# Optimization experiments

Measured on AMD Instinct MI355X. Metric: run time of the kernel, lower is better.

The kernel has to match this reference:

```python
import jax, jax.numpy as jnp
import numpy as np
import math

E_IN, E_OUT = 512, 96
B, QL, PL = 64, 128, 196

def _lin(k, shape):
    fan_in = shape[1]
    bound = 1.0 / math.sqrt(fan_in)
    k1, k2 = jax.random.split(k)
    W = jax.random.uniform(k1, shape, jnp.float32, -bound, bound)
    b = jax.random.uniform(k2, (shape[0],), jnp.float32, -bound, bound)
    return W, b

def setup_inputs() -> dict:
    key = jax.random.key(0)
    ks = jax.random.split(key, 16)
    inp = {
        'z_d_cls': jax.random.normal(ks[0], (B, E_IN), jnp.float32),
        'Z_d_tok': jax.random.normal(ks[1], (B, QL, E_IN), jnp.float32),
        'z_t_cls': jax.random.normal(ks[2], (B, E_IN), jnp.float32),
        'Z_t_tok': jax.random.normal(ks[3], (B, QL, E_IN), jnp.float32),
        'z_v_cls': jax.random.normal(ks[4], (B, E_IN), jnp.float32),
        'Z_v_patch': jax.random.normal(ks[5], (B, PL, E_IN), jnp.float32),
    }
    names = ['t_cls', 'd_cls', 'v_cls', 't_tok', 'v_patch', 'tgl_q', 'tgl_k', 'tgl_v']
    for i, n in enumerate(names):
        W, b = _lin(ks[6 + i], (E_OUT, E_IN))
        inp[f'W_{n}'] = W
        inp[f'b_{n}'] = b
    inp['ln_g'] = jnp.ones((E_OUT,), jnp.float32)
    inp['ln_b'] = jnp.zeros((E_OUT,), jnp.float32)
    return inp

def _l2n(x, eps=1e-6):
    return x / jnp.maximum(jnp.linalg.norm(x, axis=-1, keepdims=True), eps)

def _proj(x, W, b):
    return x @ W.T + b

def _layer_norm(x, g, b, eps=1e-5):
    mu = jnp.mean(x, axis=-1, keepdims=True)
    var = jnp.mean((x - mu) ** 2, axis=-1, keepdims=True)
    return (x - mu) / jnp.sqrt(var + eps) * g + b

def reference(z_d_cls, Z_d_tok, z_t_cls, Z_t_tok, z_v_cls, Z_v_patch,
              W_t_cls, b_t_cls, W_d_cls, b_d_cls, W_v_cls, b_v_cls,
              W_t_tok, b_t_tok, W_v_patch, b_v_patch,
              W_tgl_q, b_tgl_q, W_tgl_k, b_tgl_k, W_tgl_v, b_tgl_v,
              ln_g, ln_b):
    # --- TGG: global-global text/doc cosine sim [B, B]
    t = _l2n(_proj(z_t_cls, W_t_cls, b_t_cls))
    d = _l2n(_proj(z_d_cls, W_d_cls, b_d_cls))
    S_TGG = t @ d.T
    # --- TGL: cross-attention over all batch pairs
    Q = _proj(Z_d_tok, W_tgl_q, b_tgl_q)   # [b, q, h]
    K = _proj(Z_t_tok, W_tgl_k, b_tgl_k)   # [c, k, h]
    V = _proj(Z_t_tok, W_tgl_v, b_tgl_v)   # [c, k, h]
    scores = jnp.einsum('bqh,ckh->bcqk', Q, K) / math.sqrt(E_OUT)
    attn = jax.nn.softmax(scores, axis=-1)
    context = jnp.einsum('bcqk,ckh->bcqh', attn, V).mean(axis=2)  # [b, c, h]
    context = _layer_norm(context, ln_g, ln_b)
    S_TGL = jnp.einsum('ih,ijh->ij', d, _l2n(context))
    S_TIB = 0.5 * (S_TGG + S_TGL)
    # --- CGG: global-global text/vision cosine sim
    v = _l2n(_proj(z_v_cls, W_v_cls, b_v_cls))
    S_CGG = t @ v.T
    # --- CLL: token-patch max similarity
    t_tok = _l2n(_proj(Z_t_tok, W_t_tok, b_t_tok))        # [b, t, h]
    v_pat = _l2n(_proj(Z_v_patch, W_v_patch, b_v_patch))  # [c, p, h]
    sim = jnp.einsum('bth,cph->bctp', t_tok, v_pat)
    S_CLL = sim.max(axis=(-1, -2))
    S_CAB = 0.5 * (S_CGG + S_CLL)
    return S_TIB + S_CAB
```

## Files before the change

### kernel.cpp

```cpp
#include <hip/hip_runtime.h>
#include <hip/hip_bf16.h>
#include <math.h>

typedef __bf16 bf16;
typedef __attribute__((ext_vector_type(8))) __bf16 bf16x8;
typedef __attribute__((ext_vector_type(2))) float f32x2;
typedef __attribute__((ext_vector_type(4))) float f32x4;
typedef __attribute__((ext_vector_type(4))) unsigned int uint4v;

#define MFMA16(a, b, c) __builtin_amdgcn_mfma_f32_16x16x32_bf16(a, b, c, 0, 0, 0)

#define QSCALE 0.14724450f

__device__ inline bf16x8 cvt8(const float* p) {
    f32x4 lo = *(const f32x4*)p;
    f32x4 hi = *(const f32x4*)(p + 4);
    bf16x8 r;
    r[0] = (bf16)lo[0]; r[1] = (bf16)lo[1]; r[2] = (bf16)lo[2]; r[3] = (bf16)lo[3];
    r[4] = (bf16)hi[0]; r[5] = (bf16)hi[1]; r[6] = (bf16)hi[2]; r[7] = (bf16)hi[3];
    return r;
}


struct WPtrs { const float* W[8]; };

__global__ __launch_bounds__(256) void cvtw_kernel(WPtrs wp, bf16* __restrict__ Wb) {
    int j   = blockIdx.x / 48;
    int blk = blockIdx.x - j * 48;
    int idx = (blk * 256 + threadIdx.x) * 4;
    f32x4 v = *(const f32x4*)(wp.W[j] + idx);
    bf16* dst = Wb + j * 49152 + idx;
    dst[0] = (bf16)v[0]; dst[1] = (bf16)v[1]; dst[2] = (bf16)v[2]; dst[3] = (bf16)v[3];
}


struct ProjParams {
    const float* src[8];
    const float* B[8];
    void* dst[8];
    const bf16* Wb;
};

__global__ __launch_bounds__(256) void proj_kernel(ProjParams p) {
    int g   = blockIdx.x;
    int tid = threadIdx.x;
    int w2 = tid >> 6;
    int nh = w2 & 1, kh = w2 >> 1;
    int lane = tid & 63;
    int m = lane & 15, quad = lane >> 4;

    int job = 0, base = 0;
    if (g >= 2)    { job = 1; base = 2; }
    if (g >= 4)    { job = 2; base = 4; }
    if (g >= 6)    { job = 3; base = 6; }
    if (g >= 262)  { job = 4; base = 262; }
    if (g >= 518)  { job = 5; base = 518; }
    if (g >= 774)  { job = 6; base = 774; }
    if (g >= 1030) { job = 7; base = 1030; }
    int r0 = (g - base) << 5;

    const float* X  = p.src[job];
    const bf16*  wb = p.Wb + job * 49152 + (size_t)(nh * 48 + m) * 512 + kh * 256 + quad * 8;
    const float* x0 = X + (size_t)(r0 + m) * 512 + kh * 256 + quad * 8;
    const float* x1 = x0 + 16 * 512;

    f32x4 acc[2][3] = {};
    #pragma unroll
    for (int kk = 0; kk < 256; kk += 32) {
        bf16x8 a0 = cvt8(x0 + kk);
        bf16x8 a1 = cvt8(x1 + kk);
        #pragma unroll
        for (int nt = 0; nt < 3; nt++) {
            bf16x8 b = *(const bf16x8*)(wb + nt * 8192 + kk);
            acc[0][nt] = MFMA16(a0, b, acc[0][nt]);
            acc[1][nt] = MFMA16(a1, b, acc[1][nt]);
        }
    }

    __shared__ float red[2 * 64 * 24];
    __shared__ float sx[2][2][16];
    float* myred = red + (nh * 64 + lane) * 24;
    if (kh) {
        #pragma unroll
        for (int t2 = 0; t2 < 2; t2++)
            #pragma unroll
            for (int nt = 0; nt < 3; nt++)
                *(f32x4*)(myred + (t2 * 3 + nt) * 4) = acc[t2][nt];
    }
    __syncthreads();

    bool norm = (job < 3) || (job >= 6);
    const float* Bv = p.B[job];
    if (!kh) {
        #pragma unroll
        for (int t2 = 0; t2 < 2; t2++)
            #pragma unroll
            for (int nt = 0; nt < 3; nt++) {
                f32x4 o = *(const f32x4*)(myred + (t2 * 3 + nt) * 4);
                float bb = Bv[nh * 48 + nt * 16 + m];
                acc[t2][nt][0] += o[0] + bb; acc[t2][nt][1] += o[1] + bb;
                acc[t2][nt][2] += o[2] + bb; acc[t2][nt][3] += o[3] + bb;
            }
        if (norm) {
            float ss[2][4];
            #pragma unroll
            for (int t2 = 0; t2 < 2; t2++)
                #pragma unroll
                for (int r = 0; r < 4; r++) {
                    float s = 0.0f;
                    #pragma unroll
                    for (int nt = 0; nt < 3; nt++) s += acc[t2][nt][r] * acc[t2][nt][r];
                    s += __shfl_xor(s, 1); s += __shfl_xor(s, 2);
                    s += __shfl_xor(s, 4); s += __shfl_xor(s, 8);
                    ss[t2][r] = s;
                }
            if (m == 0) {
                #pragma unroll
                for (int t2 = 0; t2 < 2; t2++)
                    #pragma unroll
                    for (int r = 0; r < 4; r++)
                        sx[nh][t2][quad * 4 + r] = ss[t2][r];
            }
        }
    }
    __syncthreads();
    if (!kh) {
        if (norm) {
            #pragma unroll
            for (int t2 = 0; t2 < 2; t2++)
                #pragma unroll
                for (int r = 0; r < 4; r++) {
                    float s = 0.0f;
                    #pragma unroll
                    for (int nt = 0; nt < 3; nt++) s += acc[t2][nt][r] * acc[t2][nt][r];
                    s += __shfl_xor(s, 1); s += __shfl_xor(s, 2);
                    s += __shfl_xor(s, 4); s += __shfl_xor(s, 8);
                    float tot = s + sx[1 - nh][t2][quad * 4 + r];
                    float inv = 1.0f / fmaxf(sqrtf(tot), 1e-6f);
                    #pragma unroll
                    for (int nt = 0; nt < 3; nt++) acc[t2][nt][r] *= inv;
                }
        } else if (job == 3) {
            #pragma unroll
            for (int t2 = 0; t2 < 2; t2++)
                #pragma unroll
                for (int nt = 0; nt < 3; nt++) {
                    acc[t2][nt][0] *= QSCALE; acc[t2][nt][1] *= QSCALE;
                    acc[t2][nt][2] *= QSCALE; acc[t2][nt][3] *= QSCALE;
                }
        }
        if (job < 3) {
            float* dst = (float*)p.dst[job];
            #pragma unroll
            for (int t2 = 0; t2 < 2; t2++)
                #pragma unroll
                for (int r = 0; r < 4; r++)
                    #pragma unroll
                    for (int nt = 0; nt < 3; nt++)
                        dst[(size_t)(r0 + t2 * 16 + quad * 4 + r) * 96 + nh * 48 + nt * 16 + m] = acc[t2][nt][r];
        } else {
            bf16* dst = (bf16*)p.dst[job];
            #pragma unroll
            for (int t2 = 0; t2 < 2; t2++)
                #pragma unroll
                for (int r = 0; r < 4; r++)
                    #pragma unroll
                    for (int nt = 0; nt < 3; nt++)
                        dst[(size_t)(r0 + t2 * 16 + quad * 4 + r) * 96 + nh * 48 + nt * 16 + m] = (bf16)acc[t2][nt][r];
        }
    }
}


__global__ __launch_bounds__(256) void attn_kernel(
    const bf16* __restrict__ Qg, const bf16* __restrict__ Kg, const bf16* __restrict__ Vg,
    float* __restrict__ Ctx)
{
    int b  = blockIdx.x >> 4;
    int cg = blockIdx.x & 15;
    int tid = threadIdx.x, lane = tid & 63, w = tid >> 6;
    int m = lane & 15, quad = lane >> 4;
    const bf16* Q = Qg + (size_t)b * (128 * 96);

    bf16x8 qa0[3], qa1[3];
    #pragma unroll
    for (int i = 0; i < 3; i++) {
        qa0[i] = *(const bf16x8*)(Q + (size_t)(w * 32 + m) * 96 + i * 32 + quad * 8);
        qa1[i] = *(const bf16x8*)(Q + (size_t)(w * 32 + 16 + m) * 96 + i * 32 + quad * 8);
    }

    __shared__ __align__(16) bf16 Klds[128 * 104];
    __shared__ float wsum4[4][128];
    __shared__ float wk[128];
    __shared__ float ctxp[4][96];

    for (int ci = 0; ci < 4; ci++) {
        int c = cg * 4 + ci;
        const bf16* K = Kg + (size_t)c * (128 * 96);
        const bf16* V = Vg + (size_t)c * (128 * 96);
        #pragma unroll
        for (int it = 0; it < 6; it++) {
            int ch = it * 256 + tid;
            int row = ch / 12, seg = ch - row * 12;
            *(uint4v*)(Klds + row * 104 + seg * 8) = *(const uint4v*)(K + ch * 8);
        }
        __syncthreads();

        f32x4 acc[2][8] = {};
        #pragma unroll
        for (int kki = 0; kki < 3; kki++) {
            #pragma unroll
            for (int nt = 0; nt < 8; nt++) {
                bf16x8 bb = *(const bf16x8*)(Klds + (nt * 16 + m) * 104 + kki * 32 + quad * 8);
                acc[0][nt] = MFMA16(qa0[kki], bb, acc[0][nt]);
                acc[1][nt] = MFMA16(qa1[kki], bb, acc[1][nt]);
            }
        }
        float wpart[8];
        #pragma unroll
        for (int nt = 0; nt < 8; nt++) wpart[nt] = 0.0f;
        #pragma unroll
        for (int mt = 0; mt < 2; mt++) {
            #pragma unroll
            for (int r = 0; r < 4; r++) {
                float tv[8]; float s = 0.0f;
                #pragma unroll
                for (int nt = 0; nt < 8; nt++) { tv[nt] = exp2f(acc[mt][nt][r]); s += tv[nt]; }
                s += __shfl_xor(s, 1); s += __shfl_xor(s, 2);
                s += __shfl_xor(s, 4); s += __shfl_xor(s, 8);
                float inv = 1.0f / s;
                #pragma unroll
                for (int nt = 0; nt < 8; nt++) wpart[nt] += tv[nt] * inv;
            }
        }
        #pragma unroll
        for (int nt = 0; nt < 8; nt++) {
            wpart[nt] += __shfl_xor(wpart[nt], 16);
            wpart[nt] += __shfl_xor(wpart[nt], 32);
        }
        if (lane < 16) {
            #pragma unroll
            for (int nt = 0; nt < 8; nt++) wsum4[w][nt * 16 + lane] = wpart[nt];
        }
        __syncthreads();
        if (tid < 128) wk[tid] = wsum4[0][tid] + wsum4[1][tid] + wsum4[2][tid] + wsum4[3][tid];
        __syncthreads();
        {
            float c0 = 0.0f, c1 = 0.0f;
            if (lane < 48) {
                #pragma unroll 4
                for (int r = 0; r < 32; r++) {
                    int k = w * 32 + r;
                    unsigned u = *(const unsigned*)(V + (size_t)k * 96 + lane * 2);
                    float lo = __uint_as_float(u << 16);
                    float hi = __uint_as_float(u & 0xffff0000u);
                    float wkk = wk[k];
                    c0 += wkk * lo; c1 += wkk * hi;
                }
                ctxp[w][lane * 2]     = c0;
                ctxp[w][lane * 2 + 1] = c1;
            }
        }
        __syncthreads();
        if (tid < 96)
            Ctx[(size_t)(b * 64 + c) * 96 + tid] =
                (ctxp[0][tid] + ctxp[1][tid] + ctxp[2][tid] + ctxp[3][tid]) * (1.0f / 128.0f);
    }
}


__global__ __launch_bounds__(256) void cll_kernel(
    const bf16* __restrict__ Tt, const bf16* __restrict__ Vp, float* __restrict__ S_CLL)
{
    int c = blockIdx.x >> 3, bg = blockIdx.x & 7;
    int tid = threadIdx.x, lane = tid & 63, w = tid >> 6;
    int m = lane & 15, quad = lane >> 4;
    const bf16* P = Vp + (size_t)c * (196 * 96);

    __shared__ __align__(16) bf16 Plds[196 * 104];
    __shared__ float red[8][4];
    for (int ch = tid; ch < 2352; ch += 256) {
        int row = ch / 12, seg = ch - row * 12;
        *(uint4v*)(Plds + row * 104 + seg * 8) = *(const uint4v*)(P + ch * 8);
    }
    int rofs[13];
    #pragma unroll
    for (int nt = 0; nt < 13; nt++) {
        int r = nt * 16 + m; if (r > 195) r = 195;
        rofs[nt] = r * 104;
    }
    __syncthreads();

    for (int bi = 0; bi < 8; bi++) {
        const bf16* T = Tt + (size_t)(bg * 8 + bi) * (128 * 96);
        f32x4 acc[2][13] = {};
        #pragma unroll
        for (int kk = 0; kk < 96; kk += 32) {
            bf16x8 a0 = *(const bf16x8*)(T + (size_t)(w * 32 + m) * 96 + kk + quad * 8);
            bf16x8 a1 = *(const bf16x8*)(T + (size_t)(w * 32 + 16 + m) * 96 + kk + quad * 8);
            #pragma unroll
            for (int nt = 0; nt < 13; nt++) {
                bf16x8 bb = *(const bf16x8*)(Plds + rofs[nt] + kk + quad * 8);
                acc[0][nt] = MFMA16(a0, bb, acc[0][nt]);
                acc[1][nt] = MFMA16(a1, bb, acc[1][nt]);
            }
        }
        float mx = -3.4e38f;
        #pragma unroll
        for (int mt = 0; mt < 2; mt++)
            #pragma unroll
            for (int nt = 0; nt < 13; nt++)
                #pragma unroll
                for (int r = 0; r < 4; r++) mx = fmaxf(mx, acc[mt][nt][r]);
        #pragma unroll
        for (int d = 1; d < 64; d <<= 1) mx = fmaxf(mx, __shfl_xor(mx, d));
        if (lane == 0) red[bi][w] = mx;
    }
    __syncthreads();
    if (tid < 8)
        S_CLL[(size_t)(bg * 8 + tid) * 64 + c] =
            fmaxf(fmaxf(red[tid][0], red[tid][1]), fmaxf(red[tid][2], red[tid][3]));
}


__global__ __launch_bounds__(256) void epi_kernel(
    const float* __restrict__ Ctx, const float* __restrict__ t, const float* __restrict__ d,
    const float* __restrict__ v, const float* __restrict__ S_CLL,
    const float* __restrict__ ln_g, const float* __restrict__ ln_b,
    float* __restrict__ out)
{
    int pr = blockIdx.x * 4 + (threadIdx.x >> 6);
    int lane = threadIdx.x & 63;
    int i = pr >> 6, j = pr & 63;
    bool act = lane < 48;

    float c0 = 0, c1 = 0, t0 = 0, t1 = 0;
    float dj0 = 0, dj1 = 0, di0 = 0, di1 = 0, v0 = 0, v1 = 0, g0 = 0, g1 = 0, bb0 = 0, bb1 = 0;
    if (act) {
        f32x2 cc  = *(const f32x2*)(Ctx + (size_t)pr * 96 + lane * 2);
        f32x2 tt  = *(const f32x2*)(t + i * 96 + lane * 2);
        f32x2 ddj = *(const f32x2*)(d + j * 96 + lane * 2);
        f32x2 ddi = *(const f32x2*)(d + i * 96 + lane * 2);
        f32x2 vv  = *(const f32x2*)(v + j * 96 + lane * 2);
        f32x2 gg  = *(const f32x2*)(ln_g + lane * 2);
        f32x2 bbv = *(const f32x2*)(ln_b + lane * 2);
        c0 = cc[0]; c1 = cc[1]; t0 = tt[0]; t1 = tt[1];
        dj0 = ddj[0]; dj1 = ddj[1]; di0 = ddi[0]; di1 = ddi[1];
        v0 = vv[0]; v1 = vv[1];
        g0 = gg[0]; g1 = gg[1]; bb0 = bbv[0]; bb1 = bbv[1];
    }
    float s = c0 + c1;
    #pragma unroll
    for (int k = 1; k < 64; k <<= 1) s += __shfl_xor(s, k);
    float mean = s * (1.0f / 96.0f);
    float e0 = act ? (c0 - mean) : 0.0f;
    float e1 = act ? (c1 - mean) : 0.0f;
    float q = e0 * e0 + e1 * e1;
    #pragma unroll
    for (int k = 1; k < 64; k <<= 1) q += __shfl_xor(q, k);
    float rstd = rsqrtf(q * (1.0f / 96.0f) + 1e-5f);
    float y0 = act ? (e0 * rstd * g0 + bb0) : 0.0f;
    float y1 = act ? (e1 * rstd * g1 + bb1) : 0.0f;
    float dot = y0 * di0 + y1 * di1;
    float ssq = y0 * y0 + y1 * y1;
    float tg  = t0 * dj0 + t1 * dj1;
    float cg  = t0 * v0 + t1 * v1;
    #pragma unroll
    for (int k = 1; k < 64; k <<= 1) {
        dot += __shfl_xor(dot, k); ssq += __shfl_xor(ssq, k);
        tg  += __shfl_xor(tg, k);  cg  += __shfl_xor(cg, k);
    }
    if (lane == 0) {
        float stgl = dot / fmaxf(sqrtf(ssq), 1e-6f);
        out[pr] = 0.5f * (tg + stgl) + 0.5f * (cg + S_CLL[pr]);
    }
}


extern "C" void kernel_launch(void* const* d_in, const int* in_sizes, int n_in,
                              void* d_out, int out_size, void* d_ws, size_t ws_size,
                              hipStream_t stream)
{
    (void)in_sizes; (void)n_in; (void)out_size; (void)ws_size;
    char* ws = (char*)d_ws;
    float* t     = (float*)(ws + 0);
    float* d     = (float*)(ws + 24576);
    float* v     = (float*)(ws + 49152);
    float* S_CLL = (float*)(ws + 90112);
    bf16* Wb = (bf16*)(ws + 106496);
    bf16* Qb = (bf16*)(ws + 892928);
    bf16* Kb = (bf16*)(ws + 892928 + 1572864);
    bf16* Vb = (bf16*)(ws + 892928 + 2 * 1572864);
    bf16* Tt = (bf16*)(ws + 892928 + 3 * 1572864);
    bf16* Vp = (bf16*)(ws + 892928 + 4 * 1572864);
    float* Ctx = (float*)(ws + 892928 + 4 * 1572864 + 2408448);

    WPtrs wp;
    wp.W[0] = (const float*)d_in[6];
    wp.W[1] = (const float*)d_in[8];
    wp.W[2] = (const float*)d_in[10];
    wp.W[3] = (const float*)d_in[16];
    wp.W[4] = (const float*)d_in[18];
    wp.W[5] = (const float*)d_in[20];
    wp.W[6] = (const float*)d_in[12];
    wp.W[7] = (const float*)d_in[14];
    hipLaunchKernelGGL(cvtw_kernel, dim3(384), dim3(256), 0, stream, wp, Wb);

    ProjParams pp;
    pp.Wb = Wb;
    pp.src[0] = (const float*)d_in[2];  pp.B[0] = (const float*)d_in[7];  pp.dst[0] = t;
    pp.src[1] = (const float*)d_in[0];  pp.B[1] = (const float*)d_in[9];  pp.dst[1] = d;
    pp.src[2] = (const float*)d_in[4];  pp.B[2] = (const float*)d_in[11]; pp.dst[2] = v;
    pp.src[3] = (const float*)d_in[1];  pp.B[3] = (const float*)d_in[17]; pp.dst[3] = Qb;
    pp.src[4] = (const float*)d_in[3];  pp.B[4] = (const float*)d_in[19]; pp.dst[4] = Kb;
    pp.src[5] = (const float*)d_in[3];  pp.B[5] = (const float*)d_in[21]; pp.dst[5] = Vb;
    pp.src[6] = (const float*)d_in[3];  pp.B[6] = (const float*)d_in[13]; pp.dst[6] = Tt;
    pp.src[7] = (const float*)d_in[5];  pp.B[7] = (const float*)d_in[15]; pp.dst[7] = Vp;
    hipLaunchKernelGGL(proj_kernel, dim3(1422), dim3(256), 0, stream, pp);

    hipLaunchKernelGGL(attn_kernel, dim3(1024), dim3(256), 0, stream,
                       (const bf16*)Qb, (const bf16*)Kb, (const bf16*)Vb, Ctx);
    hipLaunchKernelGGL(cll_kernel, dim3(512), dim3(256), 0, stream,
                       (const bf16*)Tt, (const bf16*)Vp, S_CLL);
    hipLaunchKernelGGL(epi_kernel, dim3(1024), dim3(256), 0, stream,
                       (const float*)Ctx, (const float*)t, (const float*)d, (const float*)v,
                       (const float*)S_CLL, (const float*)d_in[22], (const float*)d_in[23],
                       (float*)d_out);
}
```

Measured before the change: 260.2 us.

## Split attention grid to one block per pair and fuse epilogue into CLL kernel

The attention kernel now launches one block per (b,c) pair, 4096 blocks instead of 1024 blocks each looping over four c values. This spreads the work across more blocks to raise parallelism, at the cost of reloading Q fragments per block. The epilogue kernel is folded into the CLL kernel, so S_CLL stays in shared memory and one launch plus a global round trip is removed. Each CLL block now also does layer norm and the final combination for its eight output pairs.

```diff
diff --git a/kernel.cpp b/kernel.cpp
--- a/kernel.cpp
+++ b/kernel.cpp
@@ -176,101 +176,96 @@
     const bf16* __restrict__ Qg, const bf16* __restrict__ Kg, const bf16* __restrict__ Vg,
     float* __restrict__ Ctx)
 {
-    int b  = blockIdx.x >> 4;
-    int cg = blockIdx.x & 15;
+    int pr = blockIdx.x;
+    int b = pr >> 6, c = pr & 63;
     int tid = threadIdx.x, lane = tid & 63, w = tid >> 6;
     int m = lane & 15, quad = lane >> 4;
     const bf16* Q = Qg + (size_t)b * (128 * 96);
-
-    bf16x8 qa0[3], qa1[3];
-    #pragma unroll
-    for (int i = 0; i < 3; i++) {
-        qa0[i] = *(const bf16x8*)(Q + (size_t)(w * 32 + m) * 96 + i * 32 + quad * 8);
-        qa1[i] = *(const bf16x8*)(Q + (size_t)(w * 32 + 16 + m) * 96 + i * 32 + quad * 8);
-    }
+    const bf16* K = Kg + (size_t)c * (128 * 96);
+    const bf16* V = Vg + (size_t)c * (128 * 96);
 
     __shared__ __align__(16) bf16 Klds[128 * 104];
+    #pragma unroll
+    for (int it = 0; it < 6; it++) {
+        int ch = it * 256 + tid;
+        int row = ch / 12, seg = ch - row * 12;
+        *(uint4v*)(Klds + row * 104 + seg * 8) = *(const uint4v*)(K + ch * 8);
+    }
+    __syncthreads();
+
+    f32x4 acc[2][8] = {};
+    #pragma unroll
+    for (int kk = 0; kk < 96; kk += 32) {
+        bf16x8 a0 = *(const bf16x8*)(Q + (size_t)(w * 32 + m) * 96 + kk + quad * 8);
+        bf16x8 a1 = *(const bf16x8*)(Q + (size_t)(w * 32 + 16 + m) * 96 + kk + quad * 8);
+        #pragma unroll
+        for (int nt = 0; nt < 8; nt++) {
+            bf16x8 bb = *(const bf16x8*)(Klds + (nt * 16 + m) * 104 + kk + quad * 8);
+            acc[0][nt] = MFMA16(a0, bb, acc[0][nt]);
+            acc[1][nt] = MFMA16(a1, bb, acc[1][nt]);
+        }
+    }
+    float wpart[8];
+    #pragma unroll
+    for (int nt = 0; nt < 8; nt++) wpart[nt] = 0.0f;
+    #pragma unroll
+    for (int mt = 0; mt < 2; mt++) {
+        #pragma unroll
+        for (int r = 0; r < 4; r++) {
+            float tv[8]; float s = 0.0f;
+            #pragma unroll
+            for (int nt = 0; nt < 8; nt++) { tv[nt] = exp2f(acc[mt][nt][r]); s += tv[nt]; }
+            s += __shfl_xor(s, 1); s += __shfl_xor(s, 2);
+            s += __shfl_xor(s, 4); s += __shfl_xor(s, 8);
+            float inv = 1.0f / s;
+            #pragma unroll
+            for (int nt = 0; nt < 8; nt++) wpart[nt] += tv[nt] * inv;
+        }
+    }
+    #pragma unroll
+    for (int nt = 0; nt < 8; nt++) {
+        wpart[nt] += __shfl_xor(wpart[nt], 16);
+        wpart[nt] += __shfl_xor(wpart[nt], 32);
+    }
     __shared__ float wsum4[4][128];
     __shared__ float wk[128];
     __shared__ float ctxp[4][96];
-
-    for (int ci = 0; ci < 4; ci++) {
-        int c = cg * 4 + ci;
-        const bf16* K = Kg + (size_t)c * (128 * 96);
-        const bf16* V = Vg + (size_t)c * (128 * 96);
-        #pragma unroll
-        for (int it = 0; it < 6; it++) {
-            int ch = it * 256 + tid;
-            int row = ch / 12, seg = ch - row * 12;
-            *(uint4v*)(Klds + row * 104 + seg * 8) = *(const uint4v*)(K + ch * 8);
-        }
-        __syncthreads();
-
-        f32x4 acc[2][8] = {};
-        #pragma unroll
-        for (int kki = 0; kki < 3; kki++) {
-            #pragma unroll
-            for (int nt = 0; nt < 8; nt++) {
-                bf16x8 bb = *(const bf16x8*)(Klds + (nt * 16 + m) * 104 + kki * 32 + quad * 8);
-                acc[0][nt] = MFMA16(qa0[kki], bb, acc[0][nt]);
-                acc[1][nt] = MFMA16(qa1[kki], bb, acc[1][nt]);
+    if (lane < 16) {
+        #pragma unroll
+        for (int nt = 0; nt < 8; nt++) wsum4[w][nt * 16 + lane] = wpart[nt];
+    }
+    __syncthreads();
+    if (tid < 128) wk[tid] = wsum4[0][tid] + wsum4[1][tid] + wsum4[2][tid] + wsum4[3][tid];
+    __syncthreads();
+    {
+        float c0 = 0.0f, c1 = 0.0f;
+        if (lane < 48) {
+            #pragma unroll 4
+            for (int r = 0; r < 32; r++) {
+                int k = w * 32 + r;
+                unsigned u = *(const unsigned*)(V + (size_t)k * 96 + lane * 2);
+                float lo = __uint_as_float(u << 16);
+                float hi = __uint_as_float(u & 0xffff0000u);
+                float wkk = wk[k];
+                c0 += wkk * lo; c1 += wkk * hi;
             }
-        }
-        float wpart[8];
-        #pragma unroll
-        for (int nt = 0; nt < 8; nt++) wpart[nt] = 0.0f;
-        #pragma unroll
-        for (int mt = 0; mt < 2; mt++) {
-            #pragma unroll
-            for (int r = 0; r < 4; r++) {
-                float tv[8]; float s = 0.0f;
-                #pragma unroll
-                for (int nt = 0; nt < 8; nt++) { tv[nt] = exp2f(acc[mt][nt][r]); s += tv[nt]; }
-                s += __shfl_xor(s, 1); s += __shfl_xor(s, 2);
-                s += __shfl_xor(s, 4); s += __shfl_xor(s, 8);
-                float inv = 1.0f / s;
-                #pragma unroll
-                for (int nt = 0; nt < 8; nt++) wpart[nt] += tv[nt] * inv;
-            }
-        }
-        #pragma unroll
-        for (int nt = 0; nt < 8; nt++) {
-            wpart[nt] += __shfl_xor(wpart[nt], 16);
-            wpart[nt] += __shfl_xor(wpart[nt], 32);
-        }
-        if (lane < 16) {
-            #pragma unroll
-            for (int nt = 0; nt < 8; nt++) wsum4[w][nt * 16 + lane] = wpart[nt];
-        }
-        __syncthreads();
-        if (tid < 128) wk[tid] = wsum4[0][tid] + wsum4[1][tid] + wsum4[2][tid] + wsum4[3][tid];
-        __syncthreads();
-        {
-            float c0 = 0.0f, c1 = 0.0f;
-            if (lane < 48) {
-                #pragma unroll 4
-                for (int r = 0; r < 32; r++) {
-                    int k = w * 32 + r;
-                    unsigned u = *(const unsigned*)(V + (size_t)k * 96 + lane * 2);
-                    float lo = __uint_as_float(u << 16);
-                    float hi = __uint_as_float(u & 0xffff0000u);
-                    float wkk = wk[k];
-                    c0 += wkk * lo; c1 += wkk * hi;
-                }
-                ctxp[w][lane * 2]     = c0;
-                ctxp[w][lane * 2 + 1] = c1;
-            }
-        }
-        __syncthreads();
-        if (tid < 96)
-            Ctx[(size_t)(b * 64 + c) * 96 + tid] =
-                (ctxp[0][tid] + ctxp[1][tid] + ctxp[2][tid] + ctxp[3][tid]) * (1.0f / 128.0f);
-    }
+            ctxp[w][lane * 2]     = c0;
+            ctxp[w][lane * 2 + 1] = c1;
+        }
+    }
+    __syncthreads();
+    if (tid < 96)
+        Ctx[(size_t)pr * 96 + tid] =
+            (ctxp[0][tid] + ctxp[1][tid] + ctxp[2][tid] + ctxp[3][tid]) * (1.0f / 128.0f);
 }
 
 
 __global__ __launch_bounds__(256) void cll_kernel(
-    const bf16* __restrict__ Tt, const bf16* __restrict__ Vp, float* __restrict__ S_CLL)
+    const bf16* __restrict__ Tt, const bf16* __restrict__ Vp,
+    const float* __restrict__ Ctx, const float* __restrict__ t,
+    const float* __restrict__ d, const float* __restrict__ v,
+    const float* __restrict__ ln_g, const float* __restrict__ ln_b,
+    float* __restrict__ out)
 {
     int c = blockIdx.x >> 3, bg = blockIdx.x & 7;
     int tid = threadIdx.x, lane = tid & 63, w = tid >> 6;
@@ -313,66 +308,58 @@
                 #pragma unroll
                 for (int r = 0; r < 4; r++) mx = fmaxf(mx, acc[mt][nt][r]);
         #pragma unroll
-        for (int d = 1; d < 64; d <<= 1) mx = fmaxf(mx, __shfl_xor(mx, d));
+        for (int dd = 1; dd < 64; dd <<= 1) mx = fmaxf(mx, __shfl_xor(mx, dd));
         if (lane == 0) red[bi][w] = mx;
     }
     __syncthreads();
-    if (tid < 8)
-        S_CLL[(size_t)(bg * 8 + tid) * 64 + c] =
-            fmaxf(fmaxf(red[tid][0], red[tid][1]), fmaxf(red[tid][2], red[tid][3]));
-}
-
-
-__global__ __launch_bounds__(256) void epi_kernel(
-    const float* __restrict__ Ctx, const float* __restrict__ t, const float* __restrict__ d,
-    const float* __restrict__ v, const float* __restrict__ S_CLL,
-    const float* __restrict__ ln_g, const float* __restrict__ ln_b,
-    float* __restrict__ out)
-{
-    int pr = blockIdx.x * 4 + (threadIdx.x >> 6);
-    int lane = threadIdx.x & 63;
-    int i = pr >> 6, j = pr & 63;
-    bool act = lane < 48;
-
-    float c0 = 0, c1 = 0, t0 = 0, t1 = 0;
-    float dj0 = 0, dj1 = 0, di0 = 0, di1 = 0, v0 = 0, v1 = 0, g0 = 0, g1 = 0, bb0 = 0, bb1 = 0;
-    if (act) {
-        f32x2 cc  = *(const f32x2*)(Ctx + (size_t)pr * 96 + lane * 2);
-        f32x2 tt  = *(const f32x2*)(t + i * 96 + lane * 2);
-        f32x2 ddj = *(const f32x2*)(d + j * 96 + lane * 2);
-        f32x2 ddi = *(const f32x2*)(d + i * 96 + lane * 2);
-        f32x2 vv  = *(const f32x2*)(v + j * 96 + lane * 2);
-        f32x2 gg  = *(const f32x2*)(ln_g + lane * 2);
-        f32x2 bbv = *(const f32x2*)(ln_b + lane * 2);
-        c0 = cc[0]; c1 = cc[1]; t0 = tt[0]; t1 = tt[1];
-        dj0 = ddj[0]; dj1 = ddj[1]; di0 = ddi[0]; di1 = ddi[1];
-        v0 = vv[0]; v1 = vv[1];
-        g0 = gg[0]; g1 = gg[1]; bb0 = bbv[0]; bb1 = bbv[1];
-    }
-    float s = c0 + c1;
-    #pragma unroll
-    for (int k = 1; k < 64; k <<= 1) s += __shfl_xor(s, k);
-    float mean = s * (1.0f / 96.0f);
-    float e0 = act ? (c0 - mean) : 0.0f;
-    float e1 = act ? (c1 - mean) : 0.0f;
-    float q = e0 * e0 + e1 * e1;
-    #pragma unroll
-    for (int k = 1; k < 64; k <<= 1) q += __shfl_xor(q, k);
-    float rstd = rsqrtf(q * (1.0f / 96.0f) + 1e-5f);
-    float y0 = act ? (e0 * rstd * g0 + bb0) : 0.0f;
-    float y1 = act ? (e1 * rstd * g1 + bb1) : 0.0f;
-    float dot = y0 * di0 + y1 * di1;
-    float ssq = y0 * y0 + y1 * y1;
-    float tg  = t0 * dj0 + t1 * dj1;
-    float cg  = t0 * v0 + t1 * v1;
-    #pragma unroll
-    for (int k = 1; k < 64; k <<= 1) {
-        dot += __shfl_xor(dot, k); ssq += __shfl_xor(ssq, k);
-        tg  += __shfl_xor(tg, k);  cg  += __shfl_xor(cg, k);
-    }
-    if (lane == 0) {
-        float stgl = dot / fmaxf(sqrtf(ssq), 1e-6f);
-        out[pr] = 0.5f * (tg + stgl) + 0.5f * (cg + S_CLL[pr]);
+
+    #pragma unroll
+    for (int half = 0; half < 2; half++) {
+        int bi = w + half * 4;
+        int i  = bg * 8 + bi;
+        int pr = i * 64 + c;
+        float scll = fmaxf(fmaxf(red[bi][0], red[bi][1]), fmaxf(red[bi][2], red[bi][3]));
+        bool act = lane < 48;
+        float c0 = 0, c1 = 0, t0 = 0, t1 = 0;
+        float dj0 = 0, dj1 = 0, di0 = 0, di1 = 0, v0 = 0, v1 = 0, g0 = 0, g1 = 0, bb0 = 0, bb1 = 0;
+        if (act) {
+            f32x2 cc  = *(const f32x2*)(Ctx + (size_t)pr * 96 + lane * 2);
+            f32x2 tt  = *(const f32x2*)(t + i * 96 + lane * 2);
+            f32x2 ddj = *(const f32x2*)(d + c * 96 + lane * 2);
+            f32x2 ddi = *(const f32x2*)(d + i * 96 + lane * 2);
+            f32x2 vv  = *(const f32x2*)(v + c * 96 + lane * 2);
+            f32x2 gg  = *(const f32x2*)(ln_g + lane * 2);
+            f32x2 bbv = *(const f32x2*)(ln_b + lane * 2);
+            c0 = cc[0]; c1 = cc[1]; t0 = tt[0]; t1 = tt[1];
+            dj0 = ddj[0]; dj1 = ddj[1]; di0 = ddi[0]; di1 = ddi[1];
+            v0 = vv[0]; v1 = vv[1];
+            g0 = gg[0]; g1 = gg[1]; bb0 = bbv[0]; bb1 = bbv[1];
+        }
+        float s = c0 + c1;
+        #pragma unroll
+        for (int k = 1; k < 64; k <<= 1) s += __shfl_xor(s, k);
+        float mean = s * (1.0f / 96.0f);
+        float e0 = act ? (c0 - mean) : 0.0f;
+        float e1 = act ? (c1 - mean) : 0.0f;
+        float q = e0 * e0 + e1 * e1;
+        #pragma unroll
+        for (int k = 1; k < 64; k <<= 1) q += __shfl_xor(q, k);
+        float rstd = rsqrtf(q * (1.0f / 96.0f) + 1e-5f);
+        float y0 = act ? (e0 * rstd * g0 + bb0) : 0.0f;
+        float y1 = act ? (e1 * rstd * g1 + bb1) : 0.0f;
+        float dot = y0 * di0 + y1 * di1;
+        float ssq = y0 * y0 + y1 * y1;
+        float tg  = t0 * dj0 + t1 * dj1;
+        float cg  = t0 * v0 + t1 * v1;
+        #pragma unroll
+        for (int k = 1; k < 64; k <<= 1) {
+            dot += __shfl_xor(dot, k); ssq += __shfl_xor(ssq, k);
+            tg  += __shfl_xor(tg, k);  cg  += __shfl_xor(cg, k);
+        }
+        if (lane == 0) {
+            float stgl = dot / fmaxf(sqrtf(ssq), 1e-6f);
+            out[pr] = 0.5f * (tg + stgl) + 0.5f * (cg + scll);
+        }
     }
 }
 
@@ -386,7 +373,6 @@
     float* t     = (float*)(ws + 0);
     float* d     = (float*)(ws + 24576);
     float* v     = (float*)(ws + 49152);
-    float* S_CLL = (float*)(ws + 90112);
     bf16* Wb = (bf16*)(ws + 106496);
     bf16* Qb = (bf16*)(ws + 892928);
     bf16* Kb = (bf16*)(ws + 892928 + 1572864);
@@ -418,12 +404,10 @@
     pp.src[7] = (const float*)d_in[5];  pp.B[7] = (const float*)d_in[15]; pp.dst[7] = Vp;
     hipLaunchKernelGGL(proj_kernel, dim3(1422), dim3(256), 0, stream, pp);
 
-    hipLaunchKernelGGL(attn_kernel, dim3(1024), dim3(256), 0, stream,
+    hipLaunchKernelGGL(attn_kernel, dim3(4096), dim3(256), 0, stream,
                        (const bf16*)Qb, (const bf16*)Kb, (const bf16*)Vb, Ctx);
     hipLaunchKernelGGL(cll_kernel, dim3(512), dim3(256), 0, stream,
-                       (const bf16*)Tt, (const bf16*)Vp, S_CLL);
-    hipLaunchKernelGGL(epi_kernel, dim3(1024), dim3(256), 0, stream,
+                       (const bf16*)Tt, (const bf16*)Vp,
                        (const float*)Ctx, (const float*)t, (const float*)d, (const float*)v,
-                       (const float*)S_CLL, (const float*)d_in[22], (const float*)d_in[23],
-                       (float*)d_out);
-}
+                       (const float*)d_in[22], (const float*)d_in[23], (float*)d_out);
+}
```

Measured after the change: 238.7 us. -8.3%, faster.
